# Performance work log

Measured on AMD Instinct MI355X. Metric: run time of the kernel, lower is better.

Reference implementation:

```python
import math
import jax, jax.numpy as jnp
import numpy as np

H = 768      # hidden_size
NH = 12      # num_attention_heads
K = 3        # attention_num branches (wid = None, 2, 4)
DIV = 5.0    # gauss_divisor = 2**(attention_num-1) + 1
SFT = 1.0    # sft_factor
WIDTHS = (None, 2.0, 4.0)
B, L = 4, 1024


def _layernorm(x, s, b, eps=1e-5):
    m = jnp.mean(x, axis=-1, keepdims=True)
    v = jnp.mean((x - m) ** 2, axis=-1, keepdims=True)
    return (x - m) / jnp.sqrt(v + eps) * s + b


def _log_gauss_bias(props_len, width):
    # matches generate_gauss_weight + log(clamp_min(1e-6))
    center = jnp.arange(props_len, dtype=jnp.float32) / props_len          # (L,)
    wt = jnp.maximum(jnp.float32(width), 0.01) / DIV                       # scalar
    pos = jnp.linspace(0.0, 1.0, props_len)                                # (L,)
    g = (0.3989422804014327 / wt) * jnp.exp(-(pos[None, :] - center[:, None]) ** 2 / (2.0 * wt * wt))
    g = g / jnp.max(g, axis=-1, keepdims=True)
    return jnp.log(jnp.maximum(g, 1e-6))                                   # (L, L)


def _attn(qx, kx, vx, Wq, bq, Wk, bk, Wv, bv, bias, mask):
    Bn, Lq, D = qx.shape
    dh = D // NH
    q = (qx @ Wq + bq).reshape(Bn, Lq, NH, dh)
    k = (kx @ Wk + bk).reshape(Bn, kx.shape[1], NH, dh)
    v = (vx @ Wv + bv).reshape(Bn, vx.shape[1], NH, dh)
    s = jnp.einsum('bqhd,bkhd->bhqk', q, k) / math.sqrt(dh)
    if bias is not None:
        s = s + bias[None, None]                  # cached Gaussian log-bias
    if mask is not None:
        s = s + (1.0 - mask)[:, None, None, :] * (-10000.0)
    p = jax.nn.softmax(s, axis=-1)
    return jnp.einsum('bhqk,bkhd->bqhd', p, v).reshape(Bn, Lq, D)


def _block(x, mask, Wq, bq, Wk, bk, Wv, bv, W1, b1, W2, b2, n1s, n1b, n2s, n2b, bias):
    a = _attn(x, x, x, Wq, bq, Wk, bk, Wv, bv, bias, mask)
    x = _layernorm(x + a, n1s, n1b)
    h = jax.nn.relu(x @ W1 + b1) @ W2 + b2
    return _layernorm(x + h, n2s, n2b)


def setup_inputs():
    key = jax.random.key(0)
    ks = iter(jax.random.split(key, 64))
    def p(*sh):
        return jax.random.normal(next(ks), sh, dtype=jnp.float32) * 0.02
    inp = {}
    inp['input_tensor'] = jax.random.normal(next(ks), (B, L, H), dtype=jnp.float32)
    inp['attention_mask'] = jnp.ones((B, L), dtype=jnp.float32)
    for nm, sh in [('bWq', (K, H, H)), ('bWk', (K, H, H)), ('bWv', (K, H, H)),
                   ('bW1', (K, H, 4 * H)), ('bW2', (K, 4 * H, H)),
                   ('caWq', (H, H)), ('caWk', (H, H)), ('caWv', (H, H)),
                   ('caW1', (H, H)), ('caW2', (H, H)), ('Wl1', (H, H)), ('Wl2', (H, 1))]:
        inp[nm] = p(*sh)
    for nm, sh in [('bbq', (K, H)), ('bbk', (K, H)), ('bbv', (K, H)), ('bb1', (K, 4 * H)), ('bb2', (K, H)),
                   ('cabq', (H,)), ('cabk', (H,)), ('cabv', (H,)), ('cab1', (H,)), ('cab2', (H,)),
                   ('bl1', (H,)), ('bl2', (1,))]:
        inp[nm] = jnp.zeros(sh, dtype=jnp.float32)
    for nm, sh in [('bn1s', (K, H)), ('bn2s', (K, H)), ('bns', (H,)), ('can1s', (H,)), ('can2s', (H,))]:
        inp[nm] = jnp.ones(sh, dtype=jnp.float32)
    for nm, sh in [('bn1b', (K, H)), ('bn2b', (K, H)), ('bnb', (H,)), ('can1b', (H,)), ('can2b', (H,))]:
        inp[nm] = jnp.zeros(sh, dtype=jnp.float32)
    return inp


def reference(input_tensor, attention_mask, bWq, bbq, bWk, bbk, bWv, bbv, bW1, bb1, bW2, bb2,
              bn1s, bn1b, bn2s, bn2b, bns, bnb,
              caWq, cabq, caWk, cabk, caWv, cabv, caW1, cab1, caW2, cab2,
              can1s, can1b, can2s, can2b, Wl1, bl1, Wl2, bl2):
    Bn, Ln, _ = input_tensor.shape
    mask = attention_mask
    biases = [None if w is None else _log_gauss_bias(Ln, w) for w in WIDTHS]
    outs = []
    for i in range(K):
        o = _block(input_tensor, mask,
                   bWq[i], bbq[i], bWk[i], bbk[i], bWv[i], bbv[i],
                   bW1[i], bb1[i], bW2[i], bb2[i],
                   bn1s[i], bn1b[i], bn2s[i], bn2b[i], biases[i])
        outs.append(_layernorm(o, bns, bnb))
    oo = jnp.stack(outs, axis=-1)                                   # (B, L, H, K)
    valid = mask                                                    # (B, L)
    denom = jnp.maximum(valid.sum(axis=1, keepdims=True), 1.0)      # (B, 1)
    mean_token = (oo.mean(-1) * valid[:, :, None]).sum(axis=1, keepdims=True) / denom[:, :, None]  # (B,1,H)
    selected = mean_token  # weight_token=None, mode='global' -> global_token = mean_token
    branch_feat = jnp.transpose(oo, (0, 3, 1, 2)).reshape(Bn * K, Ln, H)
    query_token = jnp.repeat(selected, K, axis=0)                   # (B*K, 1, H)
    branch_mask = jnp.repeat(mask, K, axis=0)                       # (B*K, L)
    # CrossAttention (wid=None, FFN d_ff = H)
    a = _attn(query_token, branch_feat, branch_feat, caWq, cabq, caWk, cabk, caWv, cabv, None, branch_mask)
    q = _layernorm(query_token + a, can1s, can1b)
    t = jax.nn.relu(q @ caW1 + cab1) @ caW2 + cab2
    q = _layernorm(q + t, can2s, can2b)                             # (B*K, 1, H)
    w = q.reshape(Bn, K, H)
    w = jax.nn.relu(w @ Wl1 + bl1)
    w = (w @ Wl2 + bl2)[..., 0]                                     # (B, K)
    w = jax.nn.softmax(w / SFT, axis=-1)
    return (oo * w[:, None, None, :]).sum(axis=-1)                  # (B, L, H)
```

## Files before the change

kernel.cpp:

```cpp
#include <hip/hip_runtime.h>
#include <hip/hip_bf16.h>
#include <cstdint>

typedef __hip_bfloat16 bf16;
typedef __attribute__((ext_vector_type(8))) __bf16 bf16x8;
typedef __attribute__((ext_vector_type(4))) float f32x4;

#define NE2C ((size_t)4096 * 768)

__device__ inline float ldv(const void* __restrict__ p, size_t i, bool b){
  return b ? __bfloat162float(((const bf16*)p)[i]) : ((const float*)p)[i];
}

__device__ inline float wave_sum(float v){
  #pragma unroll
  for (int o = 1; o < 64; o <<= 1) v += __shfl_xor(v, o, 64);
  return v;
}
__device__ inline float wave_max(float v){
  #pragma unroll
  for (int o = 1; o < 64; o <<= 1) v = fmaxf(v, __shfl_xor(v, o, 64));
  return v;
}

__device__ __forceinline__ void gload_lds16(const __bf16* g, __bf16* l){
  __builtin_amdgcn_global_load_lds(
      (const __attribute__((address_space(1))) uint32_t*)g,
      (__attribute__((address_space(3))) uint32_t*)l,
      16, 0, 0);
}

__global__ void flag_kernel(const void* __restrict__ bns, int* __restrict__ flagp){
  if (threadIdx.x == 0) flagp[0] = (((const uint32_t*)bns)[0] == 0x3F800000u) ? 0 : 1;
}

__global__ __launch_bounds__(256) void cvtb_kernel(const void* __restrict__ in, __bf16* __restrict__ out,
                                                   int n, const int* __restrict__ flagp){
  const bool isb = flagp[0] != 0;
  int i = blockIdx.x * 256 + threadIdx.x;
  if (i < n) out[i] = (__bf16)ldv(in, i, isb);
}

__global__ __launch_bounds__(256) void transpose_kernel(const void* __restrict__ in, size_t in_off, size_t in_zstride,
    __bf16* __restrict__ out, size_t out_off, size_t out_zstride, int K, int N, const int* __restrict__ flagp)
{
  const bool isb = flagp[0] != 0;
  const int z = blockIdx.z;
  const size_t ioff = in_off + (size_t)z * in_zstride;
  __bf16* op = out + out_off + (size_t)z * out_zstride;
  const int n0 = blockIdx.x * 64, k0 = blockIdx.y * 64;
  __shared__ __bf16 T[64][65];
  const int cr = threadIdx.x >> 6, cc = threadIdx.x & 63;
  #pragma unroll
  for (int it = 0; it < 16; ++it) {
    int r = it * 4 + cr;
    T[r][cc] = (__bf16)ldv(in, ioff + (size_t)(k0 + r) * N + (n0 + cc), isb);
  }
  __syncthreads();
  #pragma unroll
  for (int it = 0; it < 16; ++it) {
    int r = it * 4 + cr;
    op[(size_t)(n0 + r) * K + (k0 + cc)] = T[cc][r];
  }
}

__global__ __launch_bounds__(256) void biaspack_kernel(const void* bbq, const void* bbk, const void* bbv,
    const void* bb1, const void* bb2, const void* cabk, const void* cabv,
    float* __restrict__ pool, const int* __restrict__ flagp)
{
  const bool isb = flagp[0] != 0;
  int idx = blockIdx.x * 256 + threadIdx.x;
  if (idx >= 19968) return;
  float v;
  if (idx < 6912) {
    int i = idx / 2304, rem = idx % 2304;
    int m = rem / 768, c = rem % 768;
    const void* src = (m == 0) ? bbq : ((m == 1) ? bbk : bbv);
    v = ldv(src, (size_t)i * 768 + c, isb);
  } else if (idx < 16128) v = ldv(bb1, idx - 6912, isb);
  else if (idx < 18432)   v = ldv(bb2, idx - 16128, isb);
  else if (idx < 19200)   v = ldv(cabk, idx - 18432, isb);
  else                    v = ldv(cabv, idx - 19200, isb);
  pool[idx] = v;
}

__global__ __launch_bounds__(256) void gemm_mfma_kernel(
    const __bf16* __restrict__ A, size_t a_zstride,
    const __bf16* __restrict__ WT, const float* __restrict__ biasp,
    __bf16* __restrict__ C, int M, int N, int K, int relu)
{
  const int z = blockIdx.z;
  A  += (size_t)z * a_zstride;
  WT += (size_t)z * (size_t)N * K;
  biasp += (size_t)z * N;
  C  += (size_t)z * (size_t)M * N;
  const int m0 = blockIdx.y * 128, n0 = blockIdx.x * 128;
  const int tid = threadIdx.x, w = tid >> 6, lane = tid & 63;
  const int quad = lane >> 4, r16 = lane & 15;
  const int wr = w >> 1, wc = w & 1;
  __shared__ __align__(16) __bf16 As[128 * 32];
  __shared__ __align__(16) __bf16 Bs[128 * 32];
  f32x4 acc[4][4];
  #pragma unroll
  for (int i = 0; i < 4; ++i)
    #pragma unroll
    for (int j = 0; j < 4; ++j) acc[i][j] = (f32x4){0.f, 0.f, 0.f, 0.f};

  const int srow = tid >> 2;
  const int scc  = (tid & 3) * 8;

  for (int k0 = 0; k0 < K; k0 += 32) {
    __syncthreads();
    #pragma unroll
    for (int it = 0; it < 2; ++it) {
      int row = it * 64 + srow;
      const __bf16* gA = A  + (size_t)(m0 + row) * K + k0 + scc;
      const __bf16* gB = WT + (size_t)(n0 + row) * K + k0 + scc;
      __bf16* lA = &As[(it * 256 + w * 64) * 8];
      __bf16* lB = &Bs[(it * 256 + w * 64) * 8];
      gload_lds16(gA, lA);
      gload_lds16(gB, lB);
    }
    __syncthreads();
    bf16x8 af[4], bf[4];
    #pragma unroll
    for (int mt = 0; mt < 4; ++mt) af[mt] = *(const bf16x8*)&As[(wr * 64 + mt * 16 + r16) * 32 + quad * 8];
    #pragma unroll
    for (int nt = 0; nt < 4; ++nt) bf[nt] = *(const bf16x8*)&Bs[(wc * 64 + nt * 16 + r16) * 32 + quad * 8];
    #pragma unroll
    for (int mt = 0; mt < 4; ++mt)
      #pragma unroll
      for (int nt = 0; nt < 4; ++nt)
        acc[mt][nt] = __builtin_amdgcn_mfma_f32_16x16x32_bf16(af[mt], bf[nt], acc[mt][nt], 0, 0, 0);
  }
  #pragma unroll
  for (int nt = 0; nt < 4; ++nt) {
    int col = n0 + wc * 64 + nt * 16 + r16;
    float bv = biasp[col];
    #pragma unroll
    for (int mt = 0; mt < 4; ++mt) {
      int rowb = m0 + wr * 64 + mt * 16 + quad * 4;
      #pragma unroll
      for (int reg = 0; reg < 4; ++reg) {
        float v = acc[mt][nt][reg] + bv;
        if (relu) v = fmaxf(v, 0.f);
        C[(size_t)(rowb + reg) * N + col] = (__bf16)v;
      }
    }
  }
}

__global__ __launch_bounds__(256) void gemm_small_kernel(const float* __restrict__ A, const void* __restrict__ W,
    size_t woff, const void* __restrict__ bias, size_t boff, float* __restrict__ C,
    int N, int K, int relu, const int* __restrict__ flagp)
{
  const bool isb = flagp[0] != 0;
  const int row = blockIdx.y;
  const int c = blockIdx.x * 64 + (threadIdx.x & 63);
  const int ks = threadIdx.x >> 6;
  const int klen = K >> 2;
  const float* ar = A + (size_t)row * K + ks * klen;
  const size_t wbase = woff + (size_t)ks * klen * N + c;
  float acc = 0.f;
  #pragma unroll 4
  for (int k = 0; k < klen; ++k)
    acc += ar[k] * ldv(W, wbase + (size_t)k * N, isb);
  __shared__ float red[4][64];
  red[ks][threadIdx.x & 63] = acc;
  __syncthreads();
  if (threadIdx.x < 64) {
    float v = red[0][threadIdx.x] + red[1][threadIdx.x] + red[2][threadIdx.x] + red[3][threadIdx.x];
    v += ldv(bias, boff + c, isb);
    if (relu) v = fmaxf(v, 0.f);
    C[(size_t)row * N + c] = v;
  }
}

__global__ __launch_bounds__(256) void attn_mfma_kernel(
    const __bf16* __restrict__ QKV, const void* __restrict__ mask,
    __bf16* __restrict__ Aout, const int* __restrict__ flagp)
{
  const bool isb = flagp[0] != 0;
  const int bz = blockIdx.z;
  const int b = bz & 3, br = bz >> 2;
  const __bf16* Q  = QKV + (size_t)br * 3 * NE2C;
  const __bf16* Kg = Q + NE2C;
  const __bf16* Vg = Q + 2 * NE2C;
  Aout += (size_t)br * NE2C;
  const int has_bias = br > 0;
  const float inv2wt2 = (br == 1) ? 3.125f : 0.78125f;

  const int h = blockIdx.y;
  const int tid = threadIdx.x;
  const int w = tid >> 6, lane = tid & 63;
  const int quad = lane >> 4, r16 = lane & 15;
  const int qbase = blockIdx.x * 64 + w * 16;

  __shared__ __align__(16) __bf16 Ks[64 * 72];
  __shared__ __align__(16) __bf16 Vt[64 * 72];
  __shared__ __align__(16) __bf16 Ps[4][16 * 72];

  const __bf16* qrow = Q + ((size_t)(b * 1024 + qbase + r16)) * 768 + h * 64;
  bf16x8 aq0 = *(const bf16x8*)(qrow + quad * 8);
  bf16x8 aq1 = *(const bf16x8*)(qrow + 32 + quad * 8);

  float m_r[4], l_r[4], cqr[4], dminr[4];
  f32x4 O[4];
  #pragma unroll
  for (int n = 0; n < 4; ++n) O[n] = (f32x4){0.f, 0.f, 0.f, 0.f};
  #pragma unroll
  for (int reg = 0; reg < 4; ++reg) {
    m_r[reg] = -1e30f; l_r[reg] = 0.f;
    int qg = qbase + quad * 4 + reg;
    float cq = (float)qg * (1.f / 1024.f);
    cqr[reg] = cq;
    float kst = roundf(cq * 1023.f);
    float dd = kst * (1.f / 1023.f) - cq;
    dminr[reg] = dd * dd;
  }

  const int dd = tid & 63;
  const int rb = tid >> 6;
  const int dswz = (dd >> 3) & 7;

  for (int c0 = 0; c0 < 1024; c0 += 64) {
    __syncthreads();
    #pragma unroll
    for (int it = 0; it < 2; ++it) {
      int flat = it * 256 + tid;
      int r = flat >> 3;
      int c8 = (flat & 7) * 8;
      size_t g = ((size_t)(b * 1024 + c0 + r)) * 768 + h * 64 + c8;
      *(bf16x8*)&Ks[r * 72 + c8] = *(const bf16x8*)(Kg + g);
    }
    #pragma unroll
    for (int half = 0; half < 2; ++half) {
      int r0 = rb * 16 + half * 8;
      __bf16 vv[8];
      #pragma unroll
      for (int i = 0; i < 8; ++i)
        vv[i] = Vg[((size_t)(b * 1024 + c0 + r0 + i)) * 768 + h * 64 + dd];
      int blk = (r0 >> 3) ^ dswz;
      *(bf16x8*)&Vt[dd * 72 + blk * 8] = *(const bf16x8*)vv;
    }
    __syncthreads();

    float s4[4][4], p4[4][4];
    #pragma unroll
    for (int t = 0; t < 4; ++t) {
      bf16x8 b0 = *(const bf16x8*)&Ks[(t * 16 + r16) * 72 + quad * 8];
      bf16x8 b1 = *(const bf16x8*)&Ks[(t * 16 + r16) * 72 + 32 + quad * 8];
      f32x4 accq = (f32x4){0.f, 0.f, 0.f, 0.f};
      accq = __builtin_amdgcn_mfma_f32_16x16x32_bf16(aq0, b0, accq, 0, 0, 0);
      accq = __builtin_amdgcn_mfma_f32_16x16x32_bf16(aq1, b1, accq, 0, 0, 0);
      int kk = c0 + t * 16 + r16;
      float mk = ldv(mask, (size_t)(b * 1024 + kk), isb);
      float mterm = (1.f - mk) * (-10000.f);
      float pk = (float)kk * (1.f / 1023.f);
      #pragma unroll
      for (int reg = 0; reg < 4; ++reg) {
        float v = accq[reg] * 0.125f + mterm;
        if (has_bias) {
          float dd2 = pk - cqr[reg];
          v += fmaxf(-(dd2 * dd2 - dminr[reg]) * inv2wt2, -13.815511f);
        }
        s4[t][reg] = v;
      }
    }
    #pragma unroll
    for (int reg = 0; reg < 4; ++reg) {
      float tm = fmaxf(fmaxf(s4[0][reg], s4[1][reg]), fmaxf(s4[2][reg], s4[3][reg]));
      #pragma unroll
      for (int off = 1; off < 16; off <<= 1) tm = fmaxf(tm, __shfl_xor(tm, off, 64));
      float mnew = fmaxf(m_r[reg], tm);
      float alpha = __expf(m_r[reg] - mnew);
      float rs = 0.f;
      #pragma unroll
      for (int t = 0; t < 4; ++t) { float p = __expf(s4[t][reg] - mnew); p4[t][reg] = p; rs += p; }
      #pragma unroll
      for (int off = 1; off < 16; off <<= 1) rs += __shfl_xor(rs, off, 64);
      l_r[reg] = l_r[reg] * alpha + rs;
      m_r[reg] = mnew;
      #pragma unroll
      for (int n = 0; n < 4; ++n) O[n][reg] *= alpha;
    }
    __bf16* pw = &Ps[w][0];
    #pragma unroll
    for (int t = 0; t < 4; ++t)
      #pragma unroll
      for (int reg = 0; reg < 4; ++reg)
        pw[(quad * 4 + reg) * 72 + t * 16 + r16] = (__bf16)p4[t][reg];
    bf16x8 ap0 = *(const bf16x8*)&pw[r16 * 72 + quad * 8];
    bf16x8 ap1 = *(const bf16x8*)&pw[r16 * 72 + 32 + quad * 8];
    #pragma unroll
    for (int n = 0; n < 4; ++n) {
      int dr = n * 16 + r16;
      int sw = (dr >> 3) & 7;
      bf16x8 bv0 = *(const bf16x8*)&Vt[dr * 72 + (quad ^ sw) * 8];
      bf16x8 bv1 = *(const bf16x8*)&Vt[dr * 72 + ((quad + 4) ^ sw) * 8];
      O[n] = __builtin_amdgcn_mfma_f32_16x16x32_bf16(ap0, bv0, O[n], 0, 0, 0);
      O[n] = __builtin_amdgcn_mfma_f32_16x16x32_bf16(ap1, bv1, O[n], 0, 0, 0);
    }
  }
  #pragma unroll
  for (int n = 0; n < 4; ++n)
    #pragma unroll
    for (int reg = 0; reg < 4; ++reg) {
      int qg = qbase + quad * 4 + reg;
      Aout[((size_t)(b * 1024 + qg)) * 768 + h * 64 + n * 16 + r16] = (__bf16)(O[n][reg] / l_r[reg]);
    }
}

__global__ __launch_bounds__(256) void lnb_b_kernel(const __bf16* __restrict__ x, const __bf16* __restrict__ a,
    const void* __restrict__ sc, const void* __restrict__ bi, __bf16* __restrict__ out,
    const int* __restrict__ flagp)
{
  const bool isb = flagp[0] != 0;
  const int br = blockIdx.y;
  a   += (size_t)br * NE2C;
  out += (size_t)br * NE2C;
  const size_t so = (size_t)br * 768;
  int r = blockIdx.x;
  const __bf16* xr = x + (size_t)r * 768;
  const __bf16* ar = a + (size_t)r * 768;
  int t = threadIdx.x;
  float v[3]; float s = 0.f, ss = 0.f;
  #pragma unroll
  for (int j = 0; j < 3; j++) {
    int c = t + j * 256;
    float val = (float)xr[c] + (float)ar[c];
    v[j] = val; s += val; ss += val * val;
  }
  s = wave_sum(s); ss = wave_sum(ss);
  __shared__ float sred[8];
  __shared__ float stats[2];
  int lane = t & 63, wid = t >> 6;
  if (lane == 0) { sred[wid] = s; sred[4 + wid] = ss; }
  __syncthreads();
  if (t == 0) {
    float S = sred[0] + sred[1] + sred[2] + sred[3];
    float SS = sred[4] + sred[5] + sred[6] + sred[7];
    float mean = S * (1.f / 768.f);
    float var = fmaxf(SS * (1.f / 768.f) - mean * mean, 0.f);
    stats[0] = mean; stats[1] = rsqrtf(var + 1e-5f);
  }
  __syncthreads();
  float mean = stats[0], rstd = stats[1];
  #pragma unroll
  for (int j = 0; j < 3; j++) {
    int c = t + j * 256;
    out[(size_t)r * 768 + c] = (__bf16)((v[j] - mean) * rstd * ldv(sc, so + c, isb) + ldv(bi, so + c, isb));
  }
}

__global__ __launch_bounds__(256) void lnb2_b_kernel(const __bf16* __restrict__ x, const __bf16* __restrict__ a,
    const void* __restrict__ sc1, const void* __restrict__ bi1,
    const void* __restrict__ sc2, const void* __restrict__ bi2,
    __bf16* __restrict__ out, const int* __restrict__ flagp)
{
  const bool isb = flagp[0] != 0;
  const int br = blockIdx.y;
  x   += (size_t)br * NE2C;
  a   += (size_t)br * NE2C;
  out += (size_t)br * NE2C;
  const size_t s1off = (size_t)br * 768;
  int r = blockIdx.x;
  const __bf16* xr = x + (size_t)r * 768;
  const __bf16* ar = a + (size_t)r * 768;
  int t = threadIdx.x;
  int lane = t & 63, wid = t >> 6;
  __shared__ float sred[8], stats[2], sred2[8], stats2[2];

  float v[3]; float s = 0.f, ss = 0.f;
  #pragma unroll
  for (int j = 0; j < 3; j++) {
    int c = t + j * 256;
    float val = (float)xr[c] + (float)ar[c];
    v[j] = val; s += val; ss += val * val;
  }
  s = wave_sum(s); ss = wave_sum(ss);
  if (lane == 0) { sred[wid] = s; sred[4 + wid] = ss; }
  __syncthreads();
  if (t == 0) {
    float S = sred[0] + sred[1] + sred[2] + sred[3];
    float SS = sred[4] + sred[5] + sred[6] + sred[7];
    float mean = S * (1.f / 768.f);
    float var = fmaxf(SS * (1.f / 768.f) - mean * mean, 0.f);
    stats[0] = mean; stats[1] = rsqrtf(var + 1e-5f);
  }
  __syncthreads();
  float mean = stats[0], rstd = stats[1];
  float y[3]; float s2 = 0.f, ss2 = 0.f;
  #pragma unroll
  for (int j = 0; j < 3; j++) {
    int c = t + j * 256;
    float yv = (v[j] - mean) * rstd * ldv(sc1, s1off + c, isb) + ldv(bi1, s1off + c, isb);
    yv = (float)(__bf16)yv;
    y[j] = yv; s2 += yv; ss2 += yv * yv;
  }
  s2 = wave_sum(s2); ss2 = wave_sum(ss2);
  if (lane == 0) { sred2[wid] = s2; sred2[4 + wid] = ss2; }
  __syncthreads();
  if (t == 0) {
    float S = sred2[0] + sred2[1] + sred2[2] + sred2[3];
    float SS = sred2[4] + sred2[5] + sred2[6] + sred2[7];
    float mean2 = S * (1.f / 768.f);
    float var2 = fmaxf(SS * (1.f / 768.f) - mean2 * mean2, 0.f);
    stats2[0] = mean2; stats2[1] = rsqrtf(var2 + 1e-5f);
  }
  __syncthreads();
  float mean2 = stats2[0], rstd2 = stats2[1];
  #pragma unroll
  for (int j = 0; j < 3; j++) {
    int c = t + j * 256;
    out[(size_t)r * 768 + c] = (__bf16)((y[j] - mean2) * rstd2 * ldv(sc2, c, isb) + ldv(bi2, c, isb));
  }
}

__global__ __launch_bounds__(256) void ln_kernel(const float* __restrict__ x, const float* __restrict__ a,
    const void* __restrict__ sc, size_t soff, const void* __restrict__ bi, size_t boff,
    float* __restrict__ out, int xdiv, const int* __restrict__ flagp)
{
  const bool isb = flagp[0] != 0;
  int r = blockIdx.x;
  const float* xr = x + (size_t)(xdiv > 1 ? r / xdiv : r) * 768;
  const float* ar = a ? a + (size_t)r * 768 : nullptr;
  int t = threadIdx.x;
  float v[3]; float s = 0.f, ss = 0.f;
  #pragma unroll
  for (int j = 0; j < 3; j++) {
    int c = t + j * 256;
    float val = xr[c] + (ar ? ar[c] : 0.f);
    v[j] = val; s += val; ss += val * val;
  }
  s = wave_sum(s); ss = wave_sum(ss);
  __shared__ float sred[8];
  __shared__ float stats[2];
  int lane = t & 63, wid = t >> 6;
  if (lane == 0) { sred[wid] = s; sred[4 + wid] = ss; }
  __syncthreads();
  if (t == 0) {
    float S = sred[0] + sred[1] + sred[2] + sred[3];
    float SS = sred[4] + sred[5] + sred[6] + sred[7];
    float mean = S * (1.f / 768.f);
    float var = fmaxf(SS * (1.f / 768.f) - mean * mean, 0.f);
    stats[0] = mean; stats[1] = rsqrtf(var + 1e-5f);
  }
  __syncthreads();
  float mean = stats[0], rstd = stats[1];
  #pragma unroll
  for (int j = 0; j < 3; j++) {
    int c = t + j * 256;
    out[(size_t)r * 768 + c] = (v[j] - mean) * rstd * ldv(sc, soff + c, isb) + ldv(bi, boff + c, isb);
  }
}

__global__ __launch_bounds__(256) void meantok_part_kernel(const __bf16* __restrict__ OO, const void* __restrict__ mask,
    float* __restrict__ partials, const int* __restrict__ flagp)
{
  const bool isb = flagp[0] != 0;
  const size_t NE = NE2C;
  int h = blockIdx.x * 256 + threadIdx.x;
  int b = blockIdx.y, lc = blockIdx.z;
  const __bf16* base = OO + (size_t)(b * 1024 + lc * 64) * 768 + h;
  float acc = 0.f;
  for (int l = 0; l < 64; ++l) {
    float mk = ldv(mask, (size_t)(b * 1024 + lc * 64 + l), isb);
    size_t off = (size_t)l * 768;
    acc += mk * ((float)base[off] + (float)base[off + NE] + (float)base[off + 2 * NE]);
  }
  partials[((size_t)(b * 16 + lc)) * 768 + h] = acc;
}

__global__ __launch_bounds__(256) void meantok_fin_kernel(const float* __restrict__ partials,
    const void* __restrict__ mask, float* __restrict__ mt, const int* __restrict__ flagp)
{
  const bool isb = flagp[0] != 0;
  int h = blockIdx.x * 256 + threadIdx.x;
  int b = blockIdx.y;
  int t = threadIdx.x;
  float ms = 0.f;
  for (int j = t; j < 1024; j += 256) ms += ldv(mask, (size_t)(b * 1024 + j), isb);
  ms = wave_sum(ms);
  __shared__ float sred[4];
  __shared__ float msume;
  if ((t & 63) == 0) sred[t >> 6] = ms;
  __syncthreads();
  if (t == 0) msume = fmaxf(sred[0] + sred[1] + sred[2] + sred[3], 1.f);
  __syncthreads();
  float acc = 0.f;
  #pragma unroll
  for (int lc = 0; lc < 16; ++lc) acc += partials[((size_t)(b * 16 + lc)) * 768 + h];
  mt[b * 768 + h] = acc * (1.f / 3.f) / msume;
}

__global__ __launch_bounds__(64) void crossattn_kernel(const float* __restrict__ qC, const __bf16* __restrict__ kC,
    const __bf16* __restrict__ vC, const void* __restrict__ mask, float* __restrict__ caout,
    const int* __restrict__ flagp)
{
  const bool isb = flagp[0] != 0;
  int h = blockIdx.x, i = blockIdx.y, b = blockIdx.z;
  int lane = threadIdx.x;
  __shared__ float sbuf[1024];
  __shared__ float qsh[64];
  qsh[lane] = qC[b * 768 + h * 64 + lane];
  const size_t rowbase = (size_t)(i * 4 + b) * 1024;
  const __bf16* kb = kC + rowbase * 768 + h * 64;
  float lmax = -1e30f;
  for (int j = lane; j < 1024; j += 64) {
    const __bf16* kr = kb + (size_t)j * 768;
    float s = 0.f;
    #pragma unroll
    for (int d = 0; d < 64; d++) s += qsh[d] * (float)kr[d];
    s *= 0.125f;
    float mk = ldv(mask, (size_t)(b * 1024 + j), isb);
    s += (1.0f - mk) * (-10000.0f);
    sbuf[j] = s;
    lmax = fmaxf(lmax, s);
  }
  float mm = wave_max(lmax);
  float lsum = 0.f;
  for (int j = lane; j < 1024; j += 64) {
    float p = __expf(sbuf[j] - mm);
    sbuf[j] = p;
    lsum += p;
  }
  lsum = wave_sum(lsum);
  const __bf16* vb = vC + rowbase * 768 + h * 64;
  float acc = 0.f;
  for (int j = 0; j < 1024; j++) acc += sbuf[j] * (float)vb[(size_t)j * 768 + lane];
  caout[(size_t)(b * 3 + i) * 768 + h * 64 + lane] = acc / lsum;
}

__global__ __launch_bounds__(256) void logits_kernel(const float* __restrict__ wfeat, const void* __restrict__ Wl2,
    const void* __restrict__ bl2, float* __restrict__ logits, const int* __restrict__ flagp)
{
  const bool isb = flagp[0] != 0;
  int r = blockIdx.x, t = threadIdx.x;
  float s = 0.f;
  #pragma unroll
  for (int j = 0; j < 3; j++) {
    int c = t + j * 256;
    s += wfeat[(size_t)r * 768 + c] * ldv(Wl2, c, isb);
  }
  s = wave_sum(s);
  __shared__ float sred[4];
  if ((t & 63) == 0) sred[t >> 6] = s;
  __syncthreads();
  if (t == 0) logits[r] = sred[0] + sred[1] + sred[2] + sred[3] + ldv(bl2, 0, isb);
}

__global__ void wsoftmax_kernel(const float* __restrict__ logits, float* __restrict__ w)
{
  int b = threadIdx.x;
  if (b < 4) {
    float l0 = logits[b * 3], l1 = logits[b * 3 + 1], l2 = logits[b * 3 + 2];
    float m = fmaxf(l0, fmaxf(l1, l2));
    float e0 = __expf(l0 - m), e1 = __expf(l1 - m), e2 = __expf(l2 - m);
    float inv = 1.f / (e0 + e1 + e2);
    w[b * 3] = e0 * inv; w[b * 3 + 1] = e1 * inv; w[b * 3 + 2] = e2 * inv;
  }
}

__global__ __launch_bounds__(256) void combine_kernel(const __bf16* __restrict__ OO, const float* __restrict__ w,
                                                      void* __restrict__ out, const int* __restrict__ flagp)
{
  const bool isb = flagp[0] != 0;
  const size_t NE = NE2C;
  size_t idx = (size_t)blockIdx.x * 256 + threadIdx.x;
  int b = (int)(idx / (1024 * 768));
  float w0 = w[b * 3], w1 = w[b * 3 + 1], w2 = w[b * 3 + 2];
  float v = (float)OO[idx] * w0 + (float)OO[idx + NE] * w1 + (float)OO[idx + 2 * NE] * w2;
  if (isb) ((bf16*)out)[idx] = __float2bfloat16(v);
  else     ((float*)out)[idx] = v;
}

extern "C" void kernel_launch(void* const* d_in, const int* in_sizes, int n_in,
                              void* d_out, int out_size, void* d_ws, size_t ws_size,
                              hipStream_t stream)
{
  const void* X    = d_in[0];
  const void* mask = d_in[1];
  const void* bWq  = d_in[2];
  const void* bWk  = d_in[3];
  const void* bWv  = d_in[4];
  const void* bW1  = d_in[5];
  const void* bW2  = d_in[6];
  const void* caWq = d_in[7];
  const void* caWk = d_in[8];
  const void* caWv = d_in[9];
  const void* caW1 = d_in[10];
  const void* caW2 = d_in[11];
  const void* Wl1  = d_in[12];
  const void* Wl2  = d_in[13];
  const void* bbq  = d_in[14];
  const void* bbk  = d_in[15];
  const void* bbv  = d_in[16];
  const void* bb1  = d_in[17];
  const void* bb2  = d_in[18];
  const void* cabq = d_in[19];
  const void* cabk = d_in[20];
  const void* cabv = d_in[21];
  const void* cab1 = d_in[22];
  const void* cab2 = d_in[23];
  const void* bl1  = d_in[24];
  const void* bl2  = d_in[25];
  const void* bn1s = d_in[26];
  const void* bn2s = d_in[27];
  const void* bns  = d_in[28];
  const void* can1s= d_in[29];
  const void* can2s= d_in[30];
  const void* bn1b = d_in[31];
  const void* bn2b = d_in[32];
  const void* bnb  = d_in[33];
  const void* can1b= d_in[34];
  const void* can2b= d_in[35];

  const size_t NE2 = NE2C;
  const size_t WSQ = (size_t)768 * 768;
  const size_t WSF = (size_t)768 * 3072;

  __bf16* XFb  = (__bf16*)d_ws;
  __bf16* Rb   = XFb + NE2;
  __bf16* X1   = Rb + 12 * NE2;
  __bf16* AF2  = X1 + 3 * NE2;
  __bf16* WTqkv= AF2 + 3 * NE2;
  __bf16* WT1  = WTqkv + 9 * WSQ;
  __bf16* WT2  = WT1 + 3 * WSF;
  __bf16* WTc  = WT2 + 3 * WSF;
  float*  pool = (float*)(WTc + 2 * WSQ);
  float*  mt     = pool + 19968;
  float*  qC     = mt + 3072;
  float*  caout  = qC + 3072;
  float*  q1     = caout + 9216;
  float*  t1     = q1 + 9216;
  float*  t2     = t1 + 9216;
  float*  q2     = t2 + 9216;
  float*  wfeat  = q2 + 9216;
  float*  logits = wfeat + 9216;
  float*  wsm    = logits + 16;
  int*    flagp  = (int*)(wsm + 16);
  float*  partials = (float*)(flagp + 64);
  __bf16* OO = X1;
  __bf16* kC = Rb;
  __bf16* vC = Rb + 3 * NE2;

  dim3 blk256(256);
  flag_kernel<<<dim3(1), dim3(64), 0, stream>>>(bns, flagp);
  cvtb_kernel<<<dim3((int)((NE2 + 255) / 256)), blk256, 0, stream>>>(X, XFb, (int)NE2, flagp);

  transpose_kernel<<<dim3(12, 12, 3), blk256, 0, stream>>>(bWq, 0, WSQ, WTqkv, 0 * WSQ, 3 * WSQ, 768, 768, flagp);
  transpose_kernel<<<dim3(12, 12, 3), blk256, 0, stream>>>(bWk, 0, WSQ, WTqkv, 1 * WSQ, 3 * WSQ, 768, 768, flagp);
  transpose_kernel<<<dim3(12, 12, 3), blk256, 0, stream>>>(bWv, 0, WSQ, WTqkv, 2 * WSQ, 3 * WSQ, 768, 768, flagp);
  transpose_kernel<<<dim3(48, 12, 3), blk256, 0, stream>>>(bW1, 0, WSF, WT1, 0, WSF, 768, 3072, flagp);
  transpose_kernel<<<dim3(12, 48, 3), blk256, 0, stream>>>(bW2, 0, WSF, WT2, 0, WSF, 3072, 768, flagp);
  transpose_kernel<<<dim3(12, 12, 1), blk256, 0, stream>>>(caWk, 0, 0, WTc, 0, 0, 768, 768, flagp);
  transpose_kernel<<<dim3(12, 12, 1), blk256, 0, stream>>>(caWv, 0, 0, WTc, WSQ, 0, 768, 768, flagp);
  biaspack_kernel<<<dim3(78), blk256, 0, stream>>>(bbq, bbk, bbv, bb1, bb2, cabk, cabv, pool, flagp);

  gemm_mfma_kernel<<<dim3(6, 32, 9), blk256, 0, stream>>>(XFb, 0, WTqkv, pool, Rb, 4096, 768, 768, 0);
  attn_mfma_kernel<<<dim3(16, 12, 12), blk256, 0, stream>>>(Rb, mask, AF2, flagp);
  lnb_b_kernel<<<dim3(4096, 3), blk256, 0, stream>>>(XFb, AF2, bn1s, bn1b, X1, flagp);
  gemm_mfma_kernel<<<dim3(24, 32, 3), blk256, 0, stream>>>(X1, NE2, WT1, pool + 6912, Rb, 4096, 3072, 768, 1);
  gemm_mfma_kernel<<<dim3(6, 32, 3), blk256, 0, stream>>>(Rb, 4 * NE2, WT2, pool + 16128, AF2, 4096, 768, 3072, 0);
  lnb2_b_kernel<<<dim3(4096, 3), blk256, 0, stream>>>(X1, AF2, bn2s, bn2b, bns, bnb, OO, flagp);

  meantok_part_kernel<<<dim3(3, 4, 16), blk256, 0, stream>>>(OO, mask, partials, flagp);
  meantok_fin_kernel<<<dim3(3, 4), blk256, 0, stream>>>(partials, mask, mt, flagp);
  gemm_small_kernel<<<dim3(12, 4), blk256, 0, stream>>>(mt, caWq, 0, cabq, 0, qC, 768, 768, 0, flagp);
  gemm_mfma_kernel<<<dim3(6, 96, 2), blk256, 0, stream>>>(OO, 0, WTc, pool + 18432, kC, 12288, 768, 768, 0);
  crossattn_kernel<<<dim3(12, 3, 4), dim3(64), 0, stream>>>(qC, kC, vC, mask, caout, flagp);
  ln_kernel<<<dim3(12), blk256, 0, stream>>>(mt, caout, can1s, 0, can1b, 0, q1, 3, flagp);
  gemm_small_kernel<<<dim3(12, 12), blk256, 0, stream>>>(q1, caW1, 0, cab1, 0, t1, 768, 768, 1, flagp);
  gemm_small_kernel<<<dim3(12, 12), blk256, 0, stream>>>(t1, caW2, 0, cab2, 0, t2, 768, 768, 0, flagp);
  ln_kernel<<<dim3(12), blk256, 0, stream>>>(q1, t2, can2s, 0, can2b, 0, q2, 1, flagp);
  gemm_small_kernel<<<dim3(12, 12), blk256, 0, stream>>>(q2, Wl1, 0, bl1, 0, wfeat, 768, 768, 1, flagp);
  logits_kernel<<<dim3(12), blk256, 0, stream>>>(wfeat, Wl2, bl2, logits, flagp);
  wsoftmax_kernel<<<dim3(1), dim3(64), 0, stream>>>(logits, wsm);
  combine_kernel<<<dim3((int)(NE2 / 256)), blk256, 0, stream>>>(OO, wsm, d_out, flagp);
}
```

Baseline: 989.6 us.

## Precompute Gaussian bias table, use exp2 domain, and skip softmax rescale when max stable

Adds a kernel that writes the two Gaussian log-bias matrices (already scaled into log2 units) into a scratch buffer, and the attention kernel reads them instead of computing the bias per element. Scores are folded into the exp2 domain with a fused scale, the online-softmax rescale is skipped when no row max rises past a threshold, and the row-sum shuffle reduction moves to the end. This trades arithmetic for 8 MB of extra bias reads per call and an extra launch, with a lazy-rescale risk bounded by the threshold.

Result: no change. 989.7 us (+0.0%).

```diff
diff --git a/kernel.cpp b/kernel.cpp
--- a/kernel.cpp
+++ b/kernel.cpp
@@ -1,6 +1,7 @@
 #include <hip/hip_runtime.h>
 #include <hip/hip_bf16.h>
 #include <cstdint>
+#include <cmath>
 
 typedef __hip_bfloat16 bf16;
 typedef __attribute__((ext_vector_type(8))) __bf16 bf16x8;
@@ -84,6 +85,23 @@
   pool[idx] = v;
 }
 
+__global__ __launch_bounds__(256) void gaussbias_kernel(float* __restrict__ gb)
+{
+  const int br = blockIdx.x >> 10;
+  const int q  = blockIdx.x & 1023;
+  const float inv2wt2 = (br == 0) ? 3.125f : 0.78125f;
+  const float c2 = inv2wt2 * 1.4426950408889634f;
+  const float cq = (float)q * (1.f / 1024.f);
+  const float kst = roundf(cq * 1023.f);
+  const float dd = kst * (1.f / 1023.f) - cq;
+  const float dmin = dd * dd;
+  float* row = gb + (size_t)br * 1048576 + (size_t)q * 1024;
+  for (int j = threadIdx.x; j < 1024; j += 256) {
+    float d2 = (float)j * (1.f / 1023.f) - cq;
+    row[j] = fmaxf((dmin - d2 * d2) * c2, -19.9315686f);
+  }
+}
+
 __global__ __launch_bounds__(256) void gemm_mfma_kernel(
     const __bf16* __restrict__ A, size_t a_zstride,
     const __bf16* __restrict__ WT, const float* __restrict__ biasp,
@@ -178,6 +196,7 @@
 
 __global__ __launch_bounds__(256) void attn_mfma_kernel(
     const __bf16* __restrict__ QKV, const void* __restrict__ mask,
+    const float* __restrict__ gbias,
     __bf16* __restrict__ Aout, const int* __restrict__ flagp)
 {
   const bool isb = flagp[0] != 0;
@@ -188,7 +207,6 @@
   const __bf16* Vg = Q + 2 * NE2C;
   Aout += (size_t)br * NE2C;
   const int has_bias = br > 0;
-  const float inv2wt2 = (br == 1) ? 3.125f : 0.78125f;
 
   const int h = blockIdx.y;
   const int tid = threadIdx.x;
@@ -204,24 +222,28 @@
   bf16x8 aq0 = *(const bf16x8*)(qrow + quad * 8);
   bf16x8 aq1 = *(const bf16x8*)(qrow + 32 + quad * 8);
 
-  float m_r[4], l_r[4], cqr[4], dminr[4];
+  const float* brow[4];
+  if (has_bias) {
+    const float* gb = gbias + (size_t)(br - 1) * 1048576 + r16;
+    #pragma unroll
+    for (int reg = 0; reg < 4; ++reg)
+      brow[reg] = gb + (size_t)(qbase + quad * 4 + reg) * 1024;
+  }
+
+  float m_r[4], l_r[4];
   f32x4 O[4];
   #pragma unroll
   for (int n = 0; n < 4; ++n) O[n] = (f32x4){0.f, 0.f, 0.f, 0.f};
   #pragma unroll
-  for (int reg = 0; reg < 4; ++reg) {
-    m_r[reg] = -1e30f; l_r[reg] = 0.f;
-    int qg = qbase + quad * 4 + reg;
-    float cq = (float)qg * (1.f / 1024.f);
-    cqr[reg] = cq;
-    float kst = roundf(cq * 1023.f);
-    float dd = kst * (1.f / 1023.f) - cq;
-    dminr[reg] = dd * dd;
-  }
+  for (int reg = 0; reg < 4; ++reg) { m_r[reg] = -1e30f; l_r[reg] = 0.f; }
 
   const int dd = tid & 63;
   const int rb = tid >> 6;
   const int dswz = (dd >> 3) & 7;
+
+  const float SCL = 0.18033688f;
+  const float MBIG = 14426.9504f;
+  const float THR2 = 11.5415603f;
 
   for (int c0 = 0; c0 < 1024; c0 += 64) {
     __syncthreads();
@@ -255,34 +277,44 @@
       accq = __builtin_amdgcn_mfma_f32_16x16x32_bf16(aq1, b1, accq, 0, 0, 0);
       int kk = c0 + t * 16 + r16;
       float mk = ldv(mask, (size_t)(b * 1024 + kk), isb);
-      float mterm = (1.f - mk) * (-10000.f);
-      float pk = (float)kk * (1.f / 1023.f);
+      float mterm = fmaf(mk, MBIG, -MBIG);
+      if (has_bias) {
+        #pragma unroll
+        for (int reg = 0; reg < 4; ++reg)
+          s4[t][reg] = fmaf(accq[reg], SCL, mterm) + brow[reg][c0 + t * 16];
+      } else {
+        #pragma unroll
+        for (int reg = 0; reg < 4; ++reg)
+          s4[t][reg] = fmaf(accq[reg], SCL, mterm);
+      }
+    }
+    float tm[4];
+    #pragma unroll
+    for (int reg = 0; reg < 4; ++reg) {
+      float t0 = fmaxf(fmaxf(s4[0][reg], s4[1][reg]), fmaxf(s4[2][reg], s4[3][reg]));
+      #pragma unroll
+      for (int off = 1; off < 16; off <<= 1) t0 = fmaxf(t0, __shfl_xor(t0, off, 64));
+      tm[reg] = t0;
+    }
+    bool nosc = (tm[0] - m_r[0] <= THR2) && (tm[1] - m_r[1] <= THR2)
+             && (tm[2] - m_r[2] <= THR2) && (tm[3] - m_r[3] <= THR2);
+    if (!__all(nosc)) {
       #pragma unroll
       for (int reg = 0; reg < 4; ++reg) {
-        float v = accq[reg] * 0.125f + mterm;
-        if (has_bias) {
-          float dd2 = pk - cqr[reg];
-          v += fmaxf(-(dd2 * dd2 - dminr[reg]) * inv2wt2, -13.815511f);
-        }
-        s4[t][reg] = v;
+        float mnew = fmaxf(m_r[reg], tm[reg]);
+        float alpha = exp2f(m_r[reg] - mnew);
+        l_r[reg] *= alpha;
+        m_r[reg] = mnew;
+        #pragma unroll
+        for (int n = 0; n < 4; ++n) O[n][reg] *= alpha;
       }
     }
     #pragma unroll
     for (int reg = 0; reg < 4; ++reg) {
-      float tm = fmaxf(fmaxf(s4[0][reg], s4[1][reg]), fmaxf(s4[2][reg], s4[3][reg]));
-      #pragma unroll
-      for (int off = 1; off < 16; off <<= 1) tm = fmaxf(tm, __shfl_xor(tm, off, 64));
-      float mnew = fmaxf(m_r[reg], tm);
-      float alpha = __expf(m_r[reg] - mnew);
       float rs = 0.f;
       #pragma unroll
-      for (int t = 0; t < 4; ++t) { float p = __expf(s4[t][reg] - mnew); p4[t][reg] = p; rs += p; }
-      #pragma unroll
-      for (int off = 1; off < 16; off <<= 1) rs += __shfl_xor(rs, off, 64);
-      l_r[reg] = l_r[reg] * alpha + rs;
-      m_r[reg] = mnew;
-      #pragma unroll
-      for (int n = 0; n < 4; ++n) O[n][reg] *= alpha;
+      for (int t = 0; t < 4; ++t) { float p = exp2f(s4[t][reg] - m_r[reg]); p4[t][reg] = p; rs += p; }
+      l_r[reg] += rs;
     }
     __bf16* pw = &Ps[w][0];
     #pragma unroll
@@ -301,6 +333,13 @@
       O[n] = __builtin_amdgcn_mfma_f32_16x16x32_bf16(ap0, bv0, O[n], 0, 0, 0);
       O[n] = __builtin_amdgcn_mfma_f32_16x16x32_bf16(ap1, bv1, O[n], 0, 0, 0);
     }
+  }
+  #pragma unroll
+  for (int reg = 0; reg < 4; ++reg) {
+    float lv = l_r[reg];
+    #pragma unroll
+    for (int off = 1; off < 16; off <<= 1) lv += __shfl_xor(lv, off, 64);
+    l_r[reg] = lv;
   }
   #pragma unroll
   for (int n = 0; n < 4; ++n)
@@ -644,6 +683,7 @@
   __bf16* OO = X1;
   __bf16* kC = Rb;
   __bf16* vC = Rb + 3 * NE2;
+  float*  gb = (float*)X1;
 
   dim3 blk256(256);
   flag_kernel<<<dim3(1), dim3(64), 0, stream>>>(bns, flagp);
@@ -657,9 +697,10 @@
   transpose_kernel<<<dim3(12, 12, 1), blk256, 0, stream>>>(caWk, 0, 0, WTc, 0, 0, 768, 768, flagp);
   transpose_kernel<<<dim3(12, 12, 1), blk256, 0, stream>>>(caWv, 0, 0, WTc, WSQ, 0, 768, 768, flagp);
   biaspack_kernel<<<dim3(78), blk256, 0, stream>>>(bbq, bbk, bbv, bb1, bb2, cabk, cabv, pool, flagp);
+  gaussbias_kernel<<<dim3(2048), blk256, 0, stream>>>(gb);
 
   gemm_mfma_kernel<<<dim3(6, 32, 9), blk256, 0, stream>>>(XFb, 0, WTqkv, pool, Rb, 4096, 768, 768, 0);
-  attn_mfma_kernel<<<dim3(16, 12, 12), blk256, 0, stream>>>(Rb, mask, AF2, flagp);
+  attn_mfma_kernel<<<dim3(16, 12, 12), blk256, 0, stream>>>(Rb, mask, gb, AF2, flagp);
   lnb_b_kernel<<<dim3(4096, 3), blk256, 0, stream>>>(XFb, AF2, bn1s, bn1b, X1, flagp);
   gemm_mfma_kernel<<<dim3(24, 32, 3), blk256, 0, stream>>>(X1, NE2, WT1, pool + 6912, Rb, 4096, 3072, 768, 1);
   gemm_mfma_kernel<<<dim3(6, 32, 3), blk256, 0, stream>>>(Rb, 4 * NE2, WT2, pool + 16128, AF2, 4096, 768, 3072, 0);
```
